# Performance work log

Measured on AMD Instinct MI355X. Metric: run time of the kernel, lower is better.

## Reference

```python
import jax, jax.numpy as jnp
import numpy as np

NHEADS = 8
MIN_DEPTH = 0.5
MAX_DEPTH = 100.0


def _gather(img, xi, yi, nb, W, H):
    valid = (xi >= 0) & (xi < W) & (yi >= 0) & (yi < H)
    xc = jnp.clip(xi, 0, W - 1)
    yc = jnp.clip(yi, 0, H - 1)
    vals = img[nb, :, yc, xc]  # (N,Ho,Wo,C) - advanced idx dims come first
    return vals * valid[..., None].astype(img.dtype)


def grid_sample(img, grid, mode='bilinear'):
    # img: (N,C,H,W), grid: (N,Ho,Wo,2) in [-1,1], zeros padding, align_corners=True
    N, C, H, W = img.shape
    gx = (grid[..., 0] + 1.0) * 0.5 * (W - 1)
    gy = (grid[..., 1] + 1.0) * 0.5 * (H - 1)
    nb = jnp.arange(N)[:, None, None]
    if mode == 'nearest':
        out = _gather(img, jnp.round(gx).astype(jnp.int32), jnp.round(gy).astype(jnp.int32), nb, W, H)
    else:
        x0 = jnp.floor(gx); y0 = jnp.floor(gy)
        wx = (gx - x0)[..., None]; wy = (gy - y0)[..., None]
        x0i = x0.astype(jnp.int32); y0i = y0.astype(jnp.int32)
        g00 = _gather(img, x0i, y0i, nb, W, H)
        g01 = _gather(img, x0i + 1, y0i, nb, W, H)
        g10 = _gather(img, x0i, y0i + 1, nb, W, H)
        g11 = _gather(img, x0i + 1, y0i + 1, nb, W, H)
        out = (1 - wy) * ((1 - wx) * g00 + wx * g01) + wy * ((1 - wx) * g10 + wx * g11)
    return jnp.transpose(out, (0, 3, 1, 2))  # (N,C,Ho,Wo)


def _avg3(x):
    # 3x3 avg pool, stride 1, reflect pad 1 (output same HxW)
    xp = jnp.pad(x, ((0, 0), (0, 0), (1, 1), (1, 1)), mode='reflect')
    return jax.lax.reduce_window(xp, 0.0, jax.lax.add, (1, 1, 3, 3), (1, 1, 1, 1), 'VALID') / 9.0


def ssim_loss(x, y, C1=1e-4, C2=9e-4):
    mx, my = _avg3(x), _avg3(y)
    sx = _avg3(x * x) - mx * mx
    sy = _avg3(y * y) - my * my
    sxy = _avg3(x * y) - mx * my
    num = (2 * mx * my + C1) * (2 * sxy + C2)
    den = (mx * mx + my * my + C1) * (sx + sy + C2)
    return jnp.clip((1.0 - num / den) * 0.5, 0.0, 1.0)


def prepare_b(x):
    d, c, h, w = x.shape
    return x.transpose(0, 2, 3, 1).reshape(d, h * w, c)  # (seq=d, batch=h*w, c)


def layer_norm(x, g, b, eps=1e-5):
    m = x.mean(-1, keepdims=True)
    v = ((x - m) ** 2).mean(-1, keepdims=True)
    return (x - m) * jax.lax.rsqrt(v + eps) * g + b


def attention(q_in, kv_in, w_qkv, b_qkv, w_o, b_o):
    # q_in: (Lq,B,C), kv_in: (Lk,B,C)
    C = q_in.shape[-1]
    hd = C // NHEADS
    q = q_in @ w_qkv[:C].T + b_qkv[:C]
    kv = kv_in @ w_qkv[C:].T + b_qkv[C:]
    k, v = jnp.split(kv, 2, axis=-1)
    Lq, B = q.shape[0], q.shape[1]
    Lk = k.shape[0]
    q = (q * (hd ** -0.5)).reshape(Lq, B, NHEADS, hd)
    k = k.reshape(Lk, B, NHEADS, hd)
    v = v.reshape(Lk, B, NHEADS, hd)
    attn = jnp.einsum('wnhc,vnhc->nhwv', q, k)  # (B,H,Lq,Lk)
    p = jax.nn.softmax(attn, axis=-1)
    out = jnp.einsum('nhwv,vnhc->wnhc', p, v).reshape(Lq, B, C)
    out = out @ w_o.T + b_o
    raw = attn.sum(axis=1)  # (B,Lq,Lk)
    return out, raw


def _forward(feat1, feat2, coords, sa_in_w, sa_in_b, sa_out_w, sa_out_b, sa_ln_g, sa_ln_b,
             ca_in_w, ca_in_b, ca_out_w, ca_out_b, ca_ln_g, ca_ln_b, num_bins):
    bs, C, h, w = feat1.shape
    cg = jnp.where(coords < -1.0, -2.0, coords)
    cg = jnp.where(cg > 1.0, 2.0, cg)
    rep_feat2 = jnp.broadcast_to(feat2, (num_bins, C, h, w))
    warped = grid_sample(rep_feat2, cg, 'bilinear')  # (num_bins,C,h,w)
    ones = jnp.ones((num_bins, 1, h, w), feat1.dtype)
    warped_mask = grid_sample(ones, cg, 'nearest')
    # SSIM cost volume (no-grad side outputs)
    x = jnp.broadcast_to(feat1, warped.shape)
    ssim_volume = jax.lax.stop_gradient(ssim_loss(x, warped).mean(axis=1)[None])  # (1,num_bins,h,w)
    idx = jnp.argmin(ssim_volume, axis=1)  # (1,h,w)
    depth = jnp.exp(np.float32(np.log(MIN_DEPTH)) + np.float32(np.log(MAX_DEPTH / MIN_DEPTH)) * idx.astype(feat1.dtype) / (num_bins - 1))
    lowest_cost = 1.0 / depth
    f1 = prepare_b(feat1)   # (bs, h*w, C)
    f2 = prepare_b(warped)  # (num_bins, h*w, C)
    raw = None
    L = sa_in_w.shape[0]
    for i in range(L):
        f1n = layer_norm(f1, sa_ln_g[i], sa_ln_b[i])
        o, _ = attention(f1n, f1n, sa_in_w[i], sa_in_b[i], sa_out_w[i], sa_out_b[i])
        f1 = f1 + o
        f1n = layer_norm(f1, ca_ln_g[i], ca_ln_b[i])
        f2n = layer_norm(f2, ca_ln_g[i], ca_ln_b[i])
        o, raw = attention(f1n, f2n, ca_in_w[i], ca_in_b[i], ca_out_w[i], ca_out_b[i])
        f1 = f1 + o
    attn_weight = raw.reshape(bs, h, w, num_bins)
    return attn_weight, warped_mask, lowest_cost, ssim_volume


def setup_inputs():
    key = jax.random.key(0)
    ks = jax.random.split(key, 16)
    C, L, NB, H, W = 128, 6, 64, 48, 160
    s = 0.02
    return {
        'feat1': jax.random.normal(ks[0], (1, C, H, W), jnp.float32),
        'feat2': jax.random.normal(ks[1], (1, C, H, W), jnp.float32),
        'coords': jax.random.uniform(ks[2], (NB, H, W, 2), jnp.float32) * 2.4 - 1.2,
        'sa_in_w': jax.random.normal(ks[3], (L, 3 * C, C), jnp.float32) * s,
        'sa_in_b': jax.random.normal(ks[4], (L, 3 * C), jnp.float32) * s,
        'sa_out_w': jax.random.normal(ks[5], (L, C, C), jnp.float32) * s,
        'sa_out_b': jax.random.normal(ks[6], (L, C), jnp.float32) * s,
        'sa_ln_g': jnp.ones((L, C), jnp.float32),
        'sa_ln_b': jnp.zeros((L, C), jnp.float32),
        'ca_in_w': jax.random.normal(ks[7], (L, 3 * C, C), jnp.float32) * s,
        'ca_in_b': jax.random.normal(ks[8], (L, 3 * C), jnp.float32) * s,
        'ca_out_w': jax.random.normal(ks[9], (L, C, C), jnp.float32) * s,
        'ca_out_b': jax.random.normal(ks[10], (L, C), jnp.float32) * s,
        'ca_ln_g': jnp.ones((L, C), jnp.float32),
        'ca_ln_b': jnp.zeros((L, C), jnp.float32),
        'num_bins': NB,
    }


def reference(feat1, feat2, coords, sa_in_w, sa_in_b, sa_out_w, sa_out_b, sa_ln_g, sa_ln_b,
              ca_in_w, ca_in_b, ca_out_w, ca_out_b, ca_ln_g, ca_ln_b, num_bins):
    return _forward(feat1, feat2, coords, sa_in_w, sa_in_b, sa_out_w, sa_out_b, sa_ln_g, sa_ln_b,
                    ca_in_w, ca_in_b, ca_out_w, ca_out_b, ca_ln_g, ca_ln_b, num_bins)
```

## Files before the change

### kernel.cpp

```cpp
#include <hip/hip_runtime.h>

constexpr int kH  = 48;
constexpr int kW  = 160;
constexpr int kP  = 7680;
constexpr int kC  = 128;
constexpr int kNB = 64;
constexpr int kNH = 8;
constexpr int kNL = 6;

constexpr long long OFF_F1T = 0;
constexpr long long OFF_F2T = 983040;
constexpr long long OFF_F2  = 1966080;
constexpr long long OFF_MU  = OFF_F2 + 62914560LL;
constexpr long long OFF_SIG = OFF_MU + 491520LL;
constexpr long long OFF_WTS = OFF_SIG + 491520LL;
constexpr int WSA2 = 0;
constexpr int WQ2  = 8192;
constexpr int WKU  = 16384;
constexpr int WV2  = 24576;
constexpr int WO2  = 32768;
constexpr int BSA  = 40960;
constexpr int BQ   = 41088;
constexpr int BK   = 41216;
constexpr int BV   = 41344;
constexpr int WTS_STRIDE = 41472;

constexpr long long OUT_ATT  = 0;
constexpr long long OUT_MASK = 491520;
constexpr long long OUT_LC   = 983040;
constexpr long long OUT_SSIM = 990720;

typedef _Float16 h2v __attribute__((ext_vector_type(2)));
typedef __fp16 p2v __attribute__((ext_vector_type(2)));
typedef float f2v __attribute__((ext_vector_type(2)));
union U32H2 { unsigned u; h2v h; };
union U32P2 { unsigned u; p2v h; };

__device__ __forceinline__ float fdot2(unsigned a, unsigned b, float c) {
  U32H2 ua; ua.u = a; U32H2 ub; ub.u = b;
  return __builtin_amdgcn_fdot2(ua.h, ub.h, c, false);
}
__device__ __forceinline__ unsigned pkrtz(float a, float b) {
  U32P2 t; t.h = __builtin_amdgcn_cvt_pkrtz(a, b); return t.u;
}
__device__ __forceinline__ f2v h2f(unsigned u) {
  U32P2 t; t.u = u; f2v r; r.x = (float)t.h.x; r.y = (float)t.h.y; return r;
}
__device__ __forceinline__ unsigned short f2h(float x) {
  U32P2 t; t.h = __builtin_amdgcn_cvt_pkrtz(x, 0.f); return (unsigned short)(t.u & 0xffffu);
}
__device__ __forceinline__ void wb() {
  __asm__ __volatile__("" ::: "memory");
  __builtin_amdgcn_wave_barrier();
  __asm__ __volatile__("" ::: "memory");
}

__global__ void k_transpose(const float* __restrict__ feat1, const float* __restrict__ feat2,
                            float* __restrict__ f1t, float* __restrict__ f2t) {
  int idx = blockIdx.x * 256 + threadIdx.x;
  int pix = idx >> 7, c = idx & 127;
  f1t[idx] = feat1[c * kP + pix];
  f2t[idx] = feat2[c * kP + pix];
}

__device__ __forceinline__ float redsum128(float v, float* red2) {
#pragma unroll
  for (int off = 32; off > 0; off >>= 1) v += __shfl_xor(v, off);
  int t = threadIdx.x;
  if ((t & 63) == 0) red2[t >> 6] = v;
  __syncthreads();
  float r = red2[0] + red2[1];
  __syncthreads();
  return r;
}

__global__ __launch_bounds__(128) void k_fold(
    const float* __restrict__ saw_, const float* __restrict__ sab_,
    const float* __restrict__ sow_, const float* __restrict__ sob_,
    const float* __restrict__ slg_, const float* __restrict__ slb_,
    const float* __restrict__ caw_, const float* __restrict__ cab_,
    const float* __restrict__ clg_, const float* __restrict__ clb_,
    const float* __restrict__ cow_, float* __restrict__ wts) {
  int i = blockIdx.x >> 7, d = blockIdx.x & 127, c = threadIdx.x;
  const float* saw = saw_ + (long long)i * 384 * kC;
  const float* sab = sab_ + i * 384;
  const float* sow = sow_ + i * kC * kC;
  const float* sob = sob_ + i * kC;
  const float* slg = slg_ + i * kC;
  const float* slb = slb_ + i * kC;
  const float* caw = caw_ + (long long)i * 384 * kC;
  const float* cab = cab_ + i * 384;
  const float* clg = clg_ + i * kC;
  const float* clb = clb_ + i * kC;
  const float* cow = cow_ + i * kC * kC;
  float* WL = wts + (long long)i * WTS_STRIDE;
  __shared__ float red2[2];

  int jstd = (c >> 3) * 1024 + d * 8 + (c & 7);

  float acc = 0.f;
  for (int m = 0; m < kC; m++) acc += sow[d * kC + m] * saw[(256 + m) * kC + c];
  float t1 = redsum128(acc * slb[c] + sow[d * kC + c] * sab[256 + c], red2);
  if (c == 0) WL[BSA + d] = t1 + sob[d];
  ((unsigned short*)(WL + WSA2))[jstd] = f2h(acc * slg[c]);

  float wq = caw[d * kC + c];
  float t2 = redsum128(wq * clb[c], red2);
  if (c == 0) WL[BQ + d] = 0.25f * (t2 + cab[d]);
  ((unsigned short*)(WL + WQ2))[jstd] = f2h(0.25f * wq * clg[c]);

  float wk = caw[(kC + d) * kC + c];
  float t3 = redsum128(wk * clb[c], red2);
  if (c == 0) WL[BK + d] = t3 + cab[kC + d];
  {
    int h = d >> 4, o = d & 15;
    ((unsigned short*)(WL + WKU))[h * 2048 + c * 16 + o] = f2h(wk * clg[c]);
  }

  float wv = caw[(2 * kC + d) * kC + c];
  float t4 = redsum128(wv * clb[c], red2);
  if (c == 0) WL[BV + d] = t4 + cab[2 * kC + d];
  ((unsigned short*)(WL + WV2))[jstd] = f2h(wv * clg[c]);

  ((unsigned short*)(WL + WO2))[jstd] = f2h(cow[d * kC + c]);
}

__global__ __launch_bounds__(256) void k_warp(const float* __restrict__ f2t,
                                              const float* __restrict__ coords,
                                              float* __restrict__ F2, float* __restrict__ mu,
                                              float* __restrict__ sig, float* __restrict__ maskout) {
  int wave = threadIdx.x >> 6, lane = threadIdx.x & 63;
  int pix = blockIdx.x * 4 + wave;
  int b = blockIdx.y;
  long long bp = (long long)b * kP + pix;
  float cx = coords[bp * 2], cy = coords[bp * 2 + 1];
  cx = (cx < -1.f) ? -2.f : cx;
  cx = (cx > 1.f) ? 2.f : cx;
  cy = (cy < -1.f) ? -2.f : cy;
  cy = (cy > 1.f) ? 2.f : cy;
  float gx = (cx + 1.f) * 0.5f * (float)(kW - 1);
  float gy = (cy + 1.f) * 0.5f * (float)(kH - 1);
  float x0f = floorf(gx), y0f = floorf(gy);
  float wx = gx - x0f, wy = gy - y0f;
  int x0 = (int)x0f, y0 = (int)y0f;
  int x1 = x0 + 1, y1 = y0 + 1;
  float vx0 = (x0 >= 0 && x0 < kW) ? 1.f : 0.f;
  float vx1 = (x1 >= 0 && x1 < kW) ? 1.f : 0.f;
  float vy0 = (y0 >= 0 && y0 < kH) ? 1.f : 0.f;
  float vy1 = (y1 >= 0 && y1 < kH) ? 1.f : 0.f;
  int x0c = min(max(x0, 0), kW - 1), x1c = min(max(x1, 0), kW - 1);
  int y0c = min(max(y0, 0), kH - 1), y1c = min(max(y1, 0), kH - 1);
  float w00 = (1.f - wy) * (1.f - wx) * vx0 * vy0;
  float w01 = (1.f - wy) * wx * vx1 * vy0;
  float w10 = wy * (1.f - wx) * vx0 * vy1;
  float w11 = wy * wx * vx1 * vy1;
  const float2* r00 = (const float2*)(f2t + (y0c * kW + x0c) * kC);
  const float2* r01 = (const float2*)(f2t + (y0c * kW + x1c) * kC);
  const float2* r10 = (const float2*)(f2t + (y1c * kW + x0c) * kC);
  const float2* r11 = (const float2*)(f2t + (y1c * kW + x1c) * kC);
  float2 g00 = r00[lane], g01 = r01[lane], g10 = r10[lane], g11 = r11[lane];
  float v0 = w00 * g00.x + w01 * g01.x + w10 * g10.x + w11 * g11.x;
  float v1 = w00 * g00.y + w01 * g01.y + w10 * g10.y + w11 * g11.y;
  float s = v0 + v1, s2 = v0 * v0 + v1 * v1;
#pragma unroll
  for (int off = 32; off > 0; off >>= 1) {
    s += __shfl_xor(s, off);
    s2 += __shfl_xor(s2, off);
  }
  float m = s * (1.f / 128.f);
  float var = s2 * (1.f / 128.f) - m * m;
  float rs = rsqrtf(var + 1e-5f);
  float2 o;
  o.x = (v0 - m) * rs;
  o.y = (v1 - m) * rs;
  ((float2*)(F2 + bp * kC))[lane] = o;
  if (lane == 0) {
    mu[bp] = m;
    sig[bp] = sqrtf(var + 1e-5f);
    int xi = (int)rintf(gx), yi = (int)rintf(gy);
    maskout[bp] = (xi >= 0 && xi < kW && yi >= 0 && yi < kH) ? 1.f : 0.f;
  }
}

__global__ __launch_bounds__(256) void k_ssim(const float* __restrict__ f1t,
                                              const float* __restrict__ F2,
                                              const float* __restrict__ mu,
                                              const float* __restrict__ sig,
                                              float* __restrict__ ssimout) {
  const int lane = threadIdx.x & 63;
  const int y = blockIdx.x * 4 + (threadIdx.x >> 6);
  const int b = blockIdx.y;
  const int ym = (y == 0) ? 1 : y - 1;
  const int yp = (y == kH - 1) ? kH - 2 : y + 1;
  const long long bb = (long long)b * kP;
  const float* f1m = f1t + (ym * kW) * kC + 2 * lane;
  const float* f10 = f1t + (y * kW) * kC + 2 * lane;
  const float* f1p = f1t + (yp * kW) * kC + 2 * lane;
  const float* F2m = F2 + (bb + ym * kW) * kC + 2 * lane;
  const float* F20 = F2 + (bb + y * kW) * kC + 2 * lane;
  const float* F2p = F2 + (bb + yp * kW) * kC + 2 * lane;
  const float* mum = mu + bb + ym * kW;
  const float* mu0 = mu + bb + y * kW;
  const float* mup = mu + bb + yp * kW;
  const float* sgm = sig + bb + ym * kW;
  const float* sg0 = sig + bb + y * kW;
  const float* sgp = sig + bb + yp * kW;
  float* outrow = ssimout + bb + y * kW;

  f2v C[3][5];

  auto colsum = [&](int x, f2v* Cc) {
    f2v am = *(const f2v*)(f1m + (size_t)x * kC);
    f2v a0 = *(const f2v*)(f10 + (size_t)x * kC);
    f2v ap = *(const f2v*)(f1p + (size_t)x * kC);
    f2v fm = *(const f2v*)(F2m + (size_t)x * kC);
    f2v f0 = *(const f2v*)(F20 + (size_t)x * kC);
    f2v fp = *(const f2v*)(F2p + (size_t)x * kC);
    f2v wm = fm * sgm[x] + mum[x];
    f2v w0 = f0 * sg0[x] + mu0[x];
    f2v wp = fp * sgp[x] + mup[x];
    Cc[0] = am + a0 + ap;
    Cc[1] = wm + w0 + wp;
    Cc[2] = am * am + a0 * a0 + ap * ap;
    Cc[3] = wm * wm + w0 * w0 + wp * wp;
    Cc[4] = am * wm + a0 * w0 + ap * wp;
  };

  auto emit = [&](int xo, f2v s0, f2v s1, f2v s2, f2v s3, f2v s4) {
    const float inv9 = 1.f / 9.f;
    f2v mx = s0 * inv9, my = s1 * inv9;
    f2v vx = s2 * inv9 - mx * mx;
    f2v vy = s3 * inv9 - my * my;
    f2v vxy = s4 * inv9 - mx * my;
    f2v num = (2.f * mx * my + 1e-4f) * (2.f * vxy + 9e-4f);
    f2v den = (mx * mx + my * my + 1e-4f) * (vx + vy + 9e-4f);
    f2v val = (1.f - num / den) * 0.5f;
    float t = fminf(fmaxf(val.x, 0.f), 1.f) + fminf(fmaxf(val.y, 0.f), 1.f);
#pragma unroll
    for (int o = 32; o > 0; o >>= 1) t += __shfl_xor(t, o);
    if (lane == 0) outrow[xo] = t * (1.f / 128.f);
  };

  colsum(0, C[0]);
  colsum(1, C[1]);
  emit(0, C[0][0] + 2.f * C[1][0], C[0][1] + 2.f * C[1][1], C[0][2] + 2.f * C[1][2],
       C[0][3] + 2.f * C[1][3], C[0][4] + 2.f * C[1][4]);
#pragma unroll 3
  for (int x = 2; x < kW; ++x) {
    colsum(x, C[x % 3]);
    emit(x - 1, C[0][0] + C[1][0] + C[2][0], C[0][1] + C[1][1] + C[2][1],
         C[0][2] + C[1][2] + C[2][2], C[0][3] + C[1][3] + C[2][3],
         C[0][4] + C[1][4] + C[2][4]);
  }
  emit(kW - 1, C[0][0] + 2.f * C[2][0], C[0][1] + 2.f * C[2][1], C[0][2] + 2.f * C[2][2],
       C[0][3] + 2.f * C[2][3], C[0][4] + 2.f * C[2][4]);
}

__global__ __launch_bounds__(256) void k_argmin(const float* __restrict__ ssim,
                                                float* __restrict__ lc) {
  int pix = blockIdx.x * 256 + threadIdx.x;
  float best = ssim[pix];
  int bi = 0;
  for (int b = 1; b < kNB; b++) {
    float v = ssim[b * kP + pix];
    if (v < best) { best = v; bi = b; }
  }
  float depth = expf(-0.69314718f + (5.2983174f * (float)bi) / 63.0f);
  lc[pix] = 1.f / depth;
}


__device__ __forceinline__ f2v gemmW(int l, const unsigned* __restrict__ inb,
                                     const unsigned* __restrict__ W, float b0, float b1) {
  float a0 = b0, a1 = b1, c0 = 0.f, c1 = 0.f;
  const unsigned* wp = W + l * 8;
#pragma unroll
  for (int j = 0; j < 16; j += 2) {
    uint4 inA = *(const uint4*)(inb + 4 * j);
    uint4 inB = *(const uint4*)(inb + 4 * j + 4);
    uint4 wa = *(const uint4*)(wp + j * 512);
    uint4 wc = *(const uint4*)(wp + j * 512 + 4);
    uint4 wa2 = *(const uint4*)(wp + j * 512 + 512);
    uint4 wc2 = *(const uint4*)(wp + j * 512 + 516);
    a0 = fdot2(inA.x, wa.x, a0);  a0 = fdot2(inA.y, wa.y, a0);
    a0 = fdot2(inA.z, wa.z, a0);  a0 = fdot2(inA.w, wa.w, a0);
    a1 = fdot2(inA.x, wc.x, a1);  a1 = fdot2(inA.y, wc.y, a1);
    a1 = fdot2(inA.z, wc.z, a1);  a1 = fdot2(inA.w, wc.w, a1);
    c0 = fdot2(inB.x, wa2.x, c0); c0 = fdot2(inB.y, wa2.y, c0);
    c0 = fdot2(inB.z, wa2.z, c0); c0 = fdot2(inB.w, wa2.w, c0);
    c1 = fdot2(inB.x, wc2.x, c1); c1 = fdot2(inB.y, wc2.y, c1);
    c1 = fdot2(inB.z, wc2.z, c1); c1 = fdot2(inB.w, wc2.w, c1);
  }
  f2v r; r.x = a0 + c0; r.y = a1 + c1; return r;
}

__device__ __forceinline__ void ln_store(int l, f2v X, unsigned* xhq) {
  float s = X.x + X.y, s2 = X.x * X.x + X.y * X.y;
#pragma unroll
  for (int o = 32; o > 0; o >>= 1) { s += __shfl_xor(s, o); s2 += __shfl_xor(s2, o); }
  float m = s * 0.0078125f;
  float var = s2 * 0.0078125f - m * m;
  float rs = rsqrtf(var + 1e-5f);
  xhq[l] = pkrtz((X.x - m) * rs, (X.y - m) * rs);
}

__global__ __launch_bounds__(64) void k_attn(const float* __restrict__ F2g,
                                             const float* __restrict__ f1t,
                                             const float* __restrict__ wts,
                                             const float* __restrict__ cab_out,
                                             float* __restrict__ attn_out) {
  __shared__ __align__(16) unsigned F2s[64 * 64];
  __shared__ __align__(16) unsigned upb[512];
  __shared__ __align__(16) unsigned xhq[64];

  const int l = threadIdx.x;
  const int pix = blockIdx.x;

  {
#pragma unroll 4
    for (int r = 0; r < 64; ++r) {
      float2 v = *(const float2*)(F2g + ((long long)r * kP + pix) * kC + 2 * l);
      F2s[r * 64 + (l ^ (4 * (r & 15)))] = pkrtz(v.x, v.y);
    }
  }
  f2v X;
  { float2 xv = ((const float2*)(f1t + (long long)pix * kC))[l]; X.x = xv.x; X.y = xv.y; }
  wb();

  float chsum = 0.f;
  float* pf = (float*)upb;

  for (int ly = 0; ly < kNL; ++ly) {
    const float* WL = wts + (long long)ly * WTS_STRIDE;

    ln_store(l, X, xhq);
    wb();
    {
      float2 bv = ((const float2*)(WL + BSA))[l];
      f2v o = gemmW(l, xhq, (const unsigned*)(WL + WSA2), bv.x, bv.y);
      X += o;
    }
    wb();
    ln_store(l, X, xhq);
    wb();
    f2v q;
    {
      float2 bv = ((const float2*)(WL + BQ))[l];
      q = gemmW(l, xhq, (const unsigned*)(WL + WQ2), bv.x, bv.y);
    }
    if (ly == kNL - 1) {
      float2 bk = ((const float2*)(WL + BK))[l];
      float cp = q.x * bk.x + q.y * bk.y;
#pragma unroll
      for (int o = 32; o > 0; o >>= 1) cp += __shfl_xor(cp, o);
      chsum = cp;
    }
    xhq[l] = pkrtz(q.x, q.y);
    wb();

    {
      const unsigned* KU = (const unsigned*)(WL + WKU);
#pragma unroll
      for (int h = 0; h < kNH; ++h) {
        uint4 q0 = *(const uint4*)(xhq + h * 8);
        uint4 q1 = *(const uint4*)(xhq + h * 8 + 4);
        const unsigned* w0 = KU + (h * 128 + 2 * l) * 8;
        uint4 a0 = ((const uint4*)w0)[0], a1 = ((const uint4*)w0)[1];
        uint4 b0 = ((const uint4*)w0)[2], b1 = ((const uint4*)w0)[3];
        float u0 = 0.f, u1 = 0.f, u2 = 0.f, u3 = 0.f;
        u0 = fdot2(q0.x, a0.x, u0); u0 = fdot2(q0.y, a0.y, u0);
        u0 = fdot2(q0.z, a0.z, u0); u0 = fdot2(q0.w, a0.w, u0);
        u2 = fdot2(q1.x, a1.x, u2); u2 = fdot2(q1.y, a1.y, u2);
        u2 = fdot2(q1.z, a1.z, u2); u2 = fdot2(q1.w, a1.w, u2);
        u1 = fdot2(q0.x, b0.x, u1); u1 = fdot2(q0.y, b0.y, u1);
        u1 = fdot2(q0.z, b0.z, u1); u1 = fdot2(q0.w, b0.w, u1);
        u3 = fdot2(q1.x, b1.x, u3); u3 = fdot2(q1.y, b1.y, u3);
        u3 = fdot2(q1.z, b1.z, u3); u3 = fdot2(q1.w, b1.w, u3);
        upb[h * 64 + l] = pkrtz(u0 + u2, u1 + u3);
      }
    }
    wb();

    float sc[8] = {0, 0, 0, 0, 0, 0, 0, 0};
    {
      const unsigned* f2row = F2s + l * 64;
      const int sw = 4 * (l & 15);
#pragma unroll 4
      for (int j = 0; j < 16; ++j) {
        uint4 fv = *(const uint4*)(f2row + ((4 * j) ^ sw));
#pragma unroll
        for (int h = 0; h < kNH; ++h) {
          uint4 uv = *(const uint4*)(upb + h * 64 + 4 * j);
          sc[h] = fdot2(fv.x, uv.x, sc[h]);
          sc[h] = fdot2(fv.y, uv.y, sc[h]);
          sc[h] = fdot2(fv.z, uv.z, sc[h]);
          sc[h] = fdot2(fv.w, uv.w, sc[h]);
        }
      }
    }
    if (ly == kNL - 1) {
      float r = sc[0] + sc[1] + sc[2] + sc[3] + sc[4] + sc[5] + sc[6] + sc[7] + chsum;
      attn_out[(long long)pix * 64 + l] = r;
      return;
    }
    wb();
    {
      float pv[8];
#pragma unroll
      for (int h = 0; h < kNH; ++h) {
        float mx = sc[h];
#pragma unroll
        for (int o = 32; o > 0; o >>= 1) mx = fmaxf(mx, __shfl_xor(mx, o));
        float e = __expf(sc[h] - mx);
        float sm = e;
#pragma unroll
        for (int o = 32; o > 0; o >>= 1) sm += __shfl_xor(sm, o);
        pv[h] = e / sm;
      }
      *(float4*)(pf + l * 8) = make_float4(pv[0], pv[1], pv[2], pv[3]);
      *(float4*)(pf + l * 8 + 4) = make_float4(pv[4], pv[5], pv[6], pv[7]);
    }
    wb();
    {
      const int half = l >> 5, lb = l & 31;
      f2v wA[8], wB[8];
#pragma unroll
      for (int h = 0; h < kNH; ++h) { wA[h] = (f2v)0.f; wB[h] = (f2v)0.f; }
#pragma unroll 2
      for (int t = 0; t < 32; ++t) {
        int b = half * 32 + t;
        uint2 fv = *(const uint2*)(F2s + b * 64 + ((2 * lb) ^ (4 * (b & 15))));
        f2v fA = h2f(fv.x), fB = h2f(fv.y);
        float4 pA = *(const float4*)(pf + b * 8);
        float4 pB = *(const float4*)(pf + b * 8 + 4);
        wA[0] += fA * pA.x; wB[0] += fB * pA.x;
        wA[1] += fA * pA.y; wB[1] += fB * pA.y;
        wA[2] += fA * pA.z; wB[2] += fB * pA.z;
        wA[3] += fA * pA.w; wB[3] += fB * pA.w;
        wA[4] += fA * pB.x; wB[4] += fB * pB.x;
        wA[5] += fA * pB.y; wB[5] += fB * pB.y;
        wA[6] += fA * pB.z; wB[6] += fB * pB.z;
        wA[7] += fA * pB.w; wB[7] += fB * pB.w;
      }
#pragma unroll
      for (int h = 0; h < kNH; ++h) {
        wA[h].x += __shfl_xor(wA[h].x, 32);
        wA[h].y += __shfl_xor(wA[h].y, 32);
        wB[h].x += __shfl_xor(wB[h].x, 32);
        wB[h].y += __shfl_xor(wB[h].y, 32);
      }
      wb();
#pragma unroll
      for (int hh = 0; hh < 4; ++hh) {
        int h = half * 4 + hh;
        uint2 pk;
        pk.x = pkrtz(wA[h].x, wA[h].y);
        pk.y = pkrtz(wB[h].x, wB[h].y);
        *(uint2*)(upb + h * 64 + ((2 * lb) ^ (4 * h))) = pk;
      }
    }
    wb();
    {
      const int h = l >> 3;
      const unsigned* wrow = upb + h * 64;
      const unsigned* WV = (const unsigned*)(WL + WV2) + l * 8;
      float2 bv = ((const float2*)(WL + BV))[l];
      float a0 = bv.x, a1 = bv.y, c0 = 0.f, c1 = 0.f;
      const int sw = 4 * h;
#pragma unroll
      for (int j = 0; j < 16; j += 2) {
        uint4 inA = *(const uint4*)(wrow + ((4 * j) ^ sw));
        uint4 inB = *(const uint4*)(wrow + ((4 * j + 4) ^ sw));
        uint4 wa = *(const uint4*)(WV + j * 512);
        uint4 wc = *(const uint4*)(WV + j * 512 + 4);
        uint4 wa2 = *(const uint4*)(WV + j * 512 + 512);
        uint4 wc2 = *(const uint4*)(WV + j * 512 + 516);
        a0 = fdot2(inA.x, wa.x, a0);  a0 = fdot2(inA.y, wa.y, a0);
        a0 = fdot2(inA.z, wa.z, a0);  a0 = fdot2(inA.w, wa.w, a0);
        a1 = fdot2(inA.x, wc.x, a1);  a1 = fdot2(inA.y, wc.y, a1);
        a1 = fdot2(inA.z, wc.z, a1);  a1 = fdot2(inA.w, wc.w, a1);
        c0 = fdot2(inB.x, wa2.x, c0); c0 = fdot2(inB.y, wa2.y, c0);
        c0 = fdot2(inB.z, wa2.z, c0); c0 = fdot2(inB.w, wa2.w, c0);
        c1 = fdot2(inB.x, wc2.x, c1); c1 = fdot2(inB.y, wc2.y, c1);
        c1 = fdot2(inB.z, wc2.z, c1); c1 = fdot2(inB.w, wc2.w, c1);
      }
      xhq[l] = pkrtz(a0 + c0, a1 + c1);
    }
    wb();
    {
      float2 bv = ((const float2*)(cab_out + ly * kC))[l];
      f2v o = gemmW(l, xhq, (const unsigned*)(WL + WO2), bv.x, bv.y);
      X += o;
    }
    wb();
  }
}

extern "C" void kernel_launch(void* const* d_in, const int* in_sizes, int n_in, void* d_out,
                              int out_size, void* d_ws, size_t ws_size, hipStream_t stream) {
  (void)in_sizes; (void)n_in; (void)out_size; (void)ws_size;
  const float* feat1 = (const float*)d_in[0];
  const float* feat2 = (const float*)d_in[1];
  const float* coords = (const float*)d_in[2];
  const float* sa_in_w = (const float*)d_in[3];
  const float* sa_in_b = (const float*)d_in[4];
  const float* sa_out_w = (const float*)d_in[5];
  const float* sa_out_b = (const float*)d_in[6];
  const float* sa_ln_g = (const float*)d_in[7];
  const float* sa_ln_b = (const float*)d_in[8];
  const float* ca_in_w = (const float*)d_in[9];
  const float* ca_in_b = (const float*)d_in[10];
  const float* ca_out_w = (const float*)d_in[11];
  const float* ca_out_b = (const float*)d_in[12];
  const float* ca_ln_g = (const float*)d_in[13];
  const float* ca_ln_b = (const float*)d_in[14];

  float* out = (float*)d_out;
  float* ws = (float*)d_ws;
  float* f1t = ws + OFF_F1T;
  float* f2t = ws + OFF_F2T;
  float* F2 = ws + OFF_F2;
  float* mu = ws + OFF_MU;
  float* sig = ws + OFF_SIG;
  float* wts = ws + OFF_WTS;

  float* att = out + OUT_ATT;
  float* mask = out + OUT_MASK;
  float* lc = out + OUT_LC;
  float* ssim = out + OUT_SSIM;

  k_transpose<<<3840, 256, 0, stream>>>(feat1, feat2, f1t, f2t);
  k_fold<<<kNL * 128, 128, 0, stream>>>(sa_in_w, sa_in_b, sa_out_w, sa_out_b, sa_ln_g, sa_ln_b,
                                        ca_in_w, ca_in_b, ca_ln_g, ca_ln_b, ca_out_w, wts);
  dim3 g1(1920, 64);
  k_warp<<<g1, 256, 0, stream>>>(f2t, coords, F2, mu, sig, mask);
  dim3 g2(12, 64);
  k_ssim<<<g2, 256, 0, stream>>>(f1t, F2, mu, sig, ssim);
  k_argmin<<<30, 256, 0, stream>>>(ssim, lc);
  k_attn<<<kP, 64, 0, stream>>>(F2, f1t, wts, ca_out_b, att);
}
```

Measured before the change: 789.7 us.

## Use two waves per pixel in attention kernel with one output channel per thread

The attention kernel now runs 128 threads (two waves) per pixel instead of one wave. Each thread owns a single channel instead of two, and the heads are split across the two waves for the score, softmax and weighted-sum phases. The goal is to halve the per-thread serial work and register pressure and to raise latency hiding through more waves, via launch bounds of 128 threads and 4 blocks. In exchange, the cheap intra-wave barriers become __syncthreads with shared-memory reductions for LayerNorm and the final sum, and the weight matrices are read with a different per-thread layout.

```diff
diff --git a/kernel.cpp b/kernel.cpp
--- a/kernel.cpp
+++ b/kernel.cpp
@@ -48,11 +48,6 @@
 }
 __device__ __forceinline__ unsigned short f2h(float x) {
   U32P2 t; t.h = __builtin_amdgcn_cvt_pkrtz(x, 0.f); return (unsigned short)(t.u & 0xffffu);
-}
-__device__ __forceinline__ void wb() {
-  __asm__ __volatile__("" ::: "memory");
-  __builtin_amdgcn_wave_barrier();
-  __asm__ __volatile__("" ::: "memory");
 }
 
 __global__ void k_transpose(const float* __restrict__ feat1, const float* __restrict__ feat2,
@@ -270,229 +265,187 @@
 }
 
 
-__device__ __forceinline__ f2v gemmW(int l, const unsigned* __restrict__ inb,
-                                     const unsigned* __restrict__ W, float b0, float b1) {
-  float a0 = b0, a1 = b1, c0 = 0.f, c1 = 0.f;
-  const unsigned* wp = W + l * 8;
-#pragma unroll
-  for (int j = 0; j < 16; j += 2) {
-    uint4 inA = *(const uint4*)(inb + 4 * j);
-    uint4 inB = *(const uint4*)(inb + 4 * j + 4);
-    uint4 wa = *(const uint4*)(wp + j * 512);
-    uint4 wc = *(const uint4*)(wp + j * 512 + 4);
-    uint4 wa2 = *(const uint4*)(wp + j * 512 + 512);
-    uint4 wc2 = *(const uint4*)(wp + j * 512 + 516);
-    a0 = fdot2(inA.x, wa.x, a0);  a0 = fdot2(inA.y, wa.y, a0);
-    a0 = fdot2(inA.z, wa.z, a0);  a0 = fdot2(inA.w, wa.w, a0);
-    a1 = fdot2(inA.x, wc.x, a1);  a1 = fdot2(inA.y, wc.y, a1);
-    a1 = fdot2(inA.z, wc.z, a1);  a1 = fdot2(inA.w, wc.w, a1);
-    c0 = fdot2(inB.x, wa2.x, c0); c0 = fdot2(inB.y, wa2.y, c0);
-    c0 = fdot2(inB.z, wa2.z, c0); c0 = fdot2(inB.w, wa2.w, c0);
-    c1 = fdot2(inB.x, wc2.x, c1); c1 = fdot2(inB.y, wc2.y, c1);
-    c1 = fdot2(inB.z, wc2.z, c1); c1 = fdot2(inB.w, wc2.w, c1);
-  }
-  f2v r; r.x = a0 + c0; r.y = a1 + c1; return r;
-}
-
-__device__ __forceinline__ void ln_store(int l, f2v X, unsigned* xhq) {
-  float s = X.x + X.y, s2 = X.x * X.x + X.y * X.y;
-#pragma unroll
-  for (int o = 32; o > 0; o >>= 1) { s += __shfl_xor(s, o); s2 += __shfl_xor(s2, o); }
-  float m = s * 0.0078125f;
-  float var = s2 * 0.0078125f - m * m;
-  float rs = rsqrtf(var + 1e-5f);
-  xhq[l] = pkrtz((X.x - m) * rs, (X.y - m) * rs);
-}
-
-__global__ __launch_bounds__(64) void k_attn(const float* __restrict__ F2g,
-                                             const float* __restrict__ f1t,
-                                             const float* __restrict__ wts,
-                                             const float* __restrict__ cab_out,
-                                             float* __restrict__ attn_out) {
+__device__ __forceinline__ float gemm128(const unsigned* __restrict__ xh32,
+                                         const unsigned* __restrict__ W, int d, float bias) {
+  float a0 = bias, a1 = 0.f, a2 = 0.f, a3 = 0.f;
+  const unsigned* wp = W + d * 4;
+#pragma unroll
+  for (int ch = 0; ch < 16; ++ch) {
+    uint4 wv = *(const uint4*)(wp + ch * 512);
+    uint4 xv = *(const uint4*)(xh32 + ch * 4);
+    a0 = fdot2(xv.x, wv.x, a0);
+    a1 = fdot2(xv.y, wv.y, a1);
+    a2 = fdot2(xv.z, wv.z, a2);
+    a3 = fdot2(xv.w, wv.w, a3);
+  }
+  return (a0 + a1) + (a2 + a3);
+}
+
+__global__ __launch_bounds__(128, 4) void k_attn(const float* __restrict__ F2g,
+                                                 const float* __restrict__ f1t,
+                                                 const float* __restrict__ wts,
+                                                 const float* __restrict__ cab_out,
+                                                 float* __restrict__ attn_out) {
   __shared__ __align__(16) unsigned F2s[64 * 64];
   __shared__ __align__(16) unsigned upb[512];
-  __shared__ __align__(16) unsigned xhq[64];
-
-  const int l = threadIdx.x;
+  __shared__ __align__(16) unsigned xh[64];
+  __shared__ __align__(16) unsigned q2[64];
+  __shared__ float2 redf[2];
+  __shared__ float redc[2];
+  __shared__ float rawp[128];
+
+  const int t = threadIdx.x;
+  const int w = t >> 6, l = t & 63;
   const int pix = blockIdx.x;
-
-  {
-#pragma unroll 4
-    for (int r = 0; r < 64; ++r) {
-      float2 v = *(const float2*)(F2g + ((long long)r * kP + pix) * kC + 2 * l);
-      F2s[r * 64 + (l ^ (4 * (r & 15)))] = pkrtz(v.x, v.y);
-    }
-  }
-  f2v X;
-  { float2 xv = ((const float2*)(f1t + (long long)pix * kC))[l]; X.x = xv.x; X.y = xv.y; }
-  wb();
+  unsigned short* xh16 = (unsigned short*)xh;
+  unsigned short* q16 = (unsigned short*)q2;
+  unsigned short* ub16 = (unsigned short*)upb;
+  float* pf = (float*)upb;
+
+  for (int r = w * 32; r < w * 32 + 32; ++r) {
+    float2 v = *(const float2*)(F2g + ((long long)r * kP + pix) * kC + 2 * l);
+    F2s[r * 64 + (l ^ (4 * (r & 15)))] = pkrtz(v.x, v.y);
+  }
+  float X = f1t[(long long)pix * kC + t];
+  __syncthreads();
 
   float chsum = 0.f;
-  float* pf = (float*)upb;
 
   for (int ly = 0; ly < kNL; ++ly) {
     const float* WL = wts + (long long)ly * WTS_STRIDE;
 
-    ln_store(l, X, xhq);
-    wb();
-    {
-      float2 bv = ((const float2*)(WL + BSA))[l];
-      f2v o = gemmW(l, xhq, (const unsigned*)(WL + WSA2), bv.x, bv.y);
-      X += o;
-    }
-    wb();
-    ln_store(l, X, xhq);
-    wb();
-    f2v q;
-    {
-      float2 bv = ((const float2*)(WL + BQ))[l];
-      q = gemmW(l, xhq, (const unsigned*)(WL + WQ2), bv.x, bv.y);
-    }
-    if (ly == kNL - 1) {
-      float2 bk = ((const float2*)(WL + BK))[l];
-      float cp = q.x * bk.x + q.y * bk.y;
-#pragma unroll
-      for (int o = 32; o > 0; o >>= 1) cp += __shfl_xor(cp, o);
-      chsum = cp;
-    }
-    xhq[l] = pkrtz(q.x, q.y);
-    wb();
-
+    {
+      float s = X, s2 = X * X;
+#pragma unroll
+      for (int o = 32; o > 0; o >>= 1) { s += __shfl_xor(s, o); s2 += __shfl_xor(s2, o); }
+      if (l == 0) redf[w] = make_float2(s, s2);
+      __syncthreads();
+      float2 tot = redf[0], t1 = redf[1];
+      float m = (tot.x + t1.x) * 0.0078125f;
+      float var = (tot.y + t1.y) * 0.0078125f - m * m;
+      xh16[t] = f2h((X - m) * rsqrtf(var + 1e-5f));
+      __syncthreads();
+    }
+    X += gemm128(xh, (const unsigned*)(WL + WSA2), t, WL[BSA + t]);
+    {
+      float s = X, s2 = X * X;
+#pragma unroll
+      for (int o = 32; o > 0; o >>= 1) { s += __shfl_xor(s, o); s2 += __shfl_xor(s2, o); }
+      if (l == 0) redf[w] = make_float2(s, s2);
+      __syncthreads();
+      float2 tot = redf[0], t1 = redf[1];
+      float m = (tot.x + t1.x) * 0.0078125f;
+      float var = (tot.y + t1.y) * 0.0078125f - m * m;
+      xh16[t] = f2h((X - m) * rsqrtf(var + 1e-5f));
+      __syncthreads();
+    }
+    {
+      float qv = gemm128(xh, (const unsigned*)(WL + WQ2), t, WL[BQ + t]);
+      q16[t] = f2h(qv);
+      if (ly == kNL - 1) {
+        float cp = qv * WL[BK + t];
+#pragma unroll
+        for (int o = 32; o > 0; o >>= 1) cp += __shfl_xor(cp, o);
+        if (l == 0) redc[w] = cp;
+      }
+      __syncthreads();
+      if (ly == kNL - 1) chsum = redc[0] + redc[1];
+    }
     {
       const unsigned* KU = (const unsigned*)(WL + WKU);
 #pragma unroll
       for (int h = 0; h < kNH; ++h) {
-        uint4 q0 = *(const uint4*)(xhq + h * 8);
-        uint4 q1 = *(const uint4*)(xhq + h * 8 + 4);
-        const unsigned* w0 = KU + (h * 128 + 2 * l) * 8;
-        uint4 a0 = ((const uint4*)w0)[0], a1 = ((const uint4*)w0)[1];
-        uint4 b0 = ((const uint4*)w0)[2], b1 = ((const uint4*)w0)[3];
+        uint4 w0 = *(const uint4*)(KU + h * 1024 + t * 8);
+        uint4 w1 = *(const uint4*)(KU + h * 1024 + t * 8 + 4);
+        uint4 qa = *(const uint4*)(q2 + h * 8);
+        uint4 qb = *(const uint4*)(q2 + h * 8 + 4);
         float u0 = 0.f, u1 = 0.f, u2 = 0.f, u3 = 0.f;
-        u0 = fdot2(q0.x, a0.x, u0); u0 = fdot2(q0.y, a0.y, u0);
-        u0 = fdot2(q0.z, a0.z, u0); u0 = fdot2(q0.w, a0.w, u0);
-        u2 = fdot2(q1.x, a1.x, u2); u2 = fdot2(q1.y, a1.y, u2);
-        u2 = fdot2(q1.z, a1.z, u2); u2 = fdot2(q1.w, a1.w, u2);
-        u1 = fdot2(q0.x, b0.x, u1); u1 = fdot2(q0.y, b0.y, u1);
-        u1 = fdot2(q0.z, b0.z, u1); u1 = fdot2(q0.w, b0.w, u1);
-        u3 = fdot2(q1.x, b1.x, u3); u3 = fdot2(q1.y, b1.y, u3);
-        u3 = fdot2(q1.z, b1.z, u3); u3 = fdot2(q1.w, b1.w, u3);
-        upb[h * 64 + l] = pkrtz(u0 + u2, u1 + u3);
-      }
-    }
-    wb();
-
-    float sc[8] = {0, 0, 0, 0, 0, 0, 0, 0};
+        u0 = fdot2(qa.x, w0.x, u0); u1 = fdot2(qa.y, w0.y, u1);
+        u2 = fdot2(qa.z, w0.z, u2); u3 = fdot2(qa.w, w0.w, u3);
+        u0 = fdot2(qb.x, w1.x, u0); u1 = fdot2(qb.y, w1.y, u1);
+        u2 = fdot2(qb.z, w1.z, u2); u3 = fdot2(qb.w, w1.w, u3);
+        ub16[h * 128 + t] = f2h((u0 + u1) + (u2 + u3));
+      }
+      __syncthreads();
+    }
+    float sc[4] = {0, 0, 0, 0};
     {
       const unsigned* f2row = F2s + l * 64;
       const int sw = 4 * (l & 15);
+      const int hb = 4 * w;
 #pragma unroll 4
       for (int j = 0; j < 16; ++j) {
         uint4 fv = *(const uint4*)(f2row + ((4 * j) ^ sw));
 #pragma unroll
-        for (int h = 0; h < kNH; ++h) {
-          uint4 uv = *(const uint4*)(upb + h * 64 + 4 * j);
-          sc[h] = fdot2(fv.x, uv.x, sc[h]);
-          sc[h] = fdot2(fv.y, uv.y, sc[h]);
-          sc[h] = fdot2(fv.z, uv.z, sc[h]);
-          sc[h] = fdot2(fv.w, uv.w, sc[h]);
+        for (int k = 0; k < 4; ++k) {
+          uint4 uv = *(const uint4*)(upb + (hb + k) * 64 + 4 * j);
+          sc[k] = fdot2(fv.x, uv.x, sc[k]);
+          sc[k] = fdot2(fv.y, uv.y, sc[k]);
+          sc[k] = fdot2(fv.z, uv.z, sc[k]);
+          sc[k] = fdot2(fv.w, uv.w, sc[k]);
         }
       }
     }
     if (ly == kNL - 1) {
-      float r = sc[0] + sc[1] + sc[2] + sc[3] + sc[4] + sc[5] + sc[6] + sc[7] + chsum;
-      attn_out[(long long)pix * 64 + l] = r;
+      rawp[w * 64 + l] = sc[0] + sc[1] + sc[2] + sc[3];
+      __syncthreads();
+      if (t < 64) attn_out[(long long)pix * 64 + t] = rawp[t] + rawp[64 + t] + chsum;
       return;
     }
-    wb();
-    {
-      float pv[8];
-#pragma unroll
-      for (int h = 0; h < kNH; ++h) {
-        float mx = sc[h];
+    __syncthreads();
+    {
+      float pv[4];
+#pragma unroll
+      for (int k = 0; k < 4; ++k) {
+        float mx = sc[k];
 #pragma unroll
         for (int o = 32; o > 0; o >>= 1) mx = fmaxf(mx, __shfl_xor(mx, o));
-        float e = __expf(sc[h] - mx);
+        float e = __expf(sc[k] - mx);
         float sm = e;
 #pragma unroll
         for (int o = 32; o > 0; o >>= 1) sm += __shfl_xor(sm, o);
-        pv[h] = e / sm;
-      }
-      *(float4*)(pf + l * 8) = make_float4(pv[0], pv[1], pv[2], pv[3]);
-      *(float4*)(pf + l * 8 + 4) = make_float4(pv[4], pv[5], pv[6], pv[7]);
-    }
-    wb();
-    {
-      const int half = l >> 5, lb = l & 31;
-      f2v wA[8], wB[8];
-#pragma unroll
-      for (int h = 0; h < kNH; ++h) { wA[h] = (f2v)0.f; wB[h] = (f2v)0.f; }
-#pragma unroll 2
-      for (int t = 0; t < 32; ++t) {
-        int b = half * 32 + t;
-        uint2 fv = *(const uint2*)(F2s + b * 64 + ((2 * lb) ^ (4 * (b & 15))));
-        f2v fA = h2f(fv.x), fB = h2f(fv.y);
-        float4 pA = *(const float4*)(pf + b * 8);
-        float4 pB = *(const float4*)(pf + b * 8 + 4);
-        wA[0] += fA * pA.x; wB[0] += fB * pA.x;
-        wA[1] += fA * pA.y; wB[1] += fB * pA.y;
-        wA[2] += fA * pA.z; wB[2] += fB * pA.z;
-        wA[3] += fA * pA.w; wB[3] += fB * pA.w;
-        wA[4] += fA * pB.x; wB[4] += fB * pB.x;
-        wA[5] += fA * pB.y; wB[5] += fB * pB.y;
-        wA[6] += fA * pB.z; wB[6] += fB * pB.z;
-        wA[7] += fA * pB.w; wB[7] += fB * pB.w;
-      }
-#pragma unroll
-      for (int h = 0; h < kNH; ++h) {
-        wA[h].x += __shfl_xor(wA[h].x, 32);
-        wA[h].y += __shfl_xor(wA[h].y, 32);
-        wB[h].x += __shfl_xor(wB[h].x, 32);
-        wB[h].y += __shfl_xor(wB[h].y, 32);
-      }
-      wb();
-#pragma unroll
-      for (int hh = 0; hh < 4; ++hh) {
-        int h = half * 4 + hh;
-        uint2 pk;
-        pk.x = pkrtz(wA[h].x, wA[h].y);
-        pk.y = pkrtz(wB[h].x, wB[h].y);
-        *(uint2*)(upb + h * 64 + ((2 * lb) ^ (4 * h))) = pk;
-      }
-    }
-    wb();
-    {
-      const int h = l >> 3;
-      const unsigned* wrow = upb + h * 64;
-      const unsigned* WV = (const unsigned*)(WL + WV2) + l * 8;
-      float2 bv = ((const float2*)(WL + BV))[l];
-      float a0 = bv.x, a1 = bv.y, c0 = 0.f, c1 = 0.f;
+        pv[k] = e / sm;
+      }
+      *(float4*)(pf + l * 8 + 4 * w) = make_float4(pv[0], pv[1], pv[2], pv[3]);
+    }
+    __syncthreads();
+    {
+      const int hb = 4 * w;
+      f2v acc0 = (f2v)0.f, acc1 = (f2v)0.f, acc2 = (f2v)0.f, acc3 = (f2v)0.f;
+#pragma unroll 4
+      for (int b = 0; b < 64; ++b) {
+        f2v f = h2f(F2s[b * 64 + (l ^ (4 * (b & 15)))]);
+        float4 pv = *(const float4*)(pf + b * 8 + hb);
+        acc0 += f * pv.x;
+        acc1 += f * pv.y;
+        acc2 += f * pv.z;
+        acc3 += f * pv.w;
+      }
+      __syncthreads();
+      upb[(hb + 0) * 64 + (l ^ (4 * (hb + 0)))] = pkrtz(acc0.x, acc0.y);
+      upb[(hb + 1) * 64 + (l ^ (4 * (hb + 1)))] = pkrtz(acc1.x, acc1.y);
+      upb[(hb + 2) * 64 + (l ^ (4 * (hb + 2)))] = pkrtz(acc2.x, acc2.y);
+      upb[(hb + 3) * 64 + (l ^ (4 * (hb + 3)))] = pkrtz(acc3.x, acc3.y);
+      __syncthreads();
+    }
+    {
+      const int h = t >> 4;
+      const unsigned* WV = (const unsigned*)(WL + WV2) + t * 4;
+      float a0 = WL[BV + t], a1 = 0.f, a2 = 0.f, a3 = 0.f;
       const int sw = 4 * h;
 #pragma unroll
-      for (int j = 0; j < 16; j += 2) {
-        uint4 inA = *(const uint4*)(wrow + ((4 * j) ^ sw));
-        uint4 inB = *(const uint4*)(wrow + ((4 * j + 4) ^ sw));
-        uint4 wa = *(const uint4*)(WV + j * 512);
-        uint4 wc = *(const uint4*)(WV + j * 512 + 4);
-        uint4 wa2 = *(const uint4*)(WV + j * 512 + 512);
-        uint4 wc2 = *(const uint4*)(WV + j * 512 + 516);
-        a0 = fdot2(inA.x, wa.x, a0);  a0 = fdot2(inA.y, wa.y, a0);
-        a0 = fdot2(inA.z, wa.z, a0);  a0 = fdot2(inA.w, wa.w, a0);
-        a1 = fdot2(inA.x, wc.x, a1);  a1 = fdot2(inA.y, wc.y, a1);
-        a1 = fdot2(inA.z, wc.z, a1);  a1 = fdot2(inA.w, wc.w, a1);
-        c0 = fdot2(inB.x, wa2.x, c0); c0 = fdot2(inB.y, wa2.y, c0);
-        c0 = fdot2(inB.z, wa2.z, c0); c0 = fdot2(inB.w, wa2.w, c0);
-        c1 = fdot2(inB.x, wc2.x, c1); c1 = fdot2(inB.y, wc2.y, c1);
-        c1 = fdot2(inB.z, wc2.z, c1); c1 = fdot2(inB.w, wc2.w, c1);
-      }
-      xhq[l] = pkrtz(a0 + c0, a1 + c1);
-    }
-    wb();
-    {
-      float2 bv = ((const float2*)(cab_out + ly * kC))[l];
-      f2v o = gemmW(l, xhq, (const unsigned*)(WL + WO2), bv.x, bv.y);
-      X += o;
-    }
-    wb();
+      for (int ch = 0; ch < 16; ++ch) {
+        uint4 wv = *(const uint4*)(WV + ch * 512);
+        uint4 iv = *(const uint4*)(upb + h * 64 + ((4 * ch) ^ sw));
+        a0 = fdot2(iv.x, wv.x, a0);
+        a1 = fdot2(iv.y, wv.y, a1);
+        a2 = fdot2(iv.z, wv.z, a2);
+        a3 = fdot2(iv.w, wv.w, a3);
+      }
+      xh16[t] = f2h((a0 + a1) + (a2 + a3));
+      __syncthreads();
+    }
+    X += gemm128(xh, (const unsigned*)(WL + WO2), t, cab_out[ly * kC + t]);
   }
 }
 
@@ -537,5 +490,5 @@
   dim3 g2(12, 64);
   k_ssim<<<g2, 256, 0, stream>>>(f1t, F2, mu, sig, ssim);
   k_argmin<<<30, 256, 0, stream>>>(ssim, lc);
-  k_attn<<<kP, 64, 0, stream>>>(F2, f1t, wts, ca_out_b, att);
-}
+  k_attn<<<kP, 128, 0, stream>>>(F2, f1t, wts, ca_out_b, att);
+}
```

Measured after the change: 1.044 ms. 1.32x slower.

## Compute per-head attention scores with MFMA 32x32x16 instead of fdot2 loops

Applied to the files above, without the earlier changes.

Replaces the per-lane fdot2 loop that computes the 64 bins × 8 heads score matrix with two MFMA 32x32x16 f16 instructions per K-chunk. Each lane's B column is indexed by head via mrow&7, so columns 8–31 are redundant copies. The softmax is restructured around the MFMA output layout: max and sum are reduced in registers plus one cross-half shuffle, and only lanes with mrow<8 write probabilities to shared memory. This cuts dot-product instruction count and cross-lane shuffles. In exchange, 75% of the MFMA work is wasted on duplicate columns and the result layout needs remapping through shared memory.

```diff
diff --git a/kernel.cpp b/kernel.cpp
--- a/kernel.cpp
+++ b/kernel.cpp
@@ -33,6 +33,8 @@
 typedef _Float16 h2v __attribute__((ext_vector_type(2)));
 typedef __fp16 p2v __attribute__((ext_vector_type(2)));
 typedef float f2v __attribute__((ext_vector_type(2)));
+typedef __fp16 h8 __attribute__((ext_vector_type(8)));
+typedef float fx16 __attribute__((ext_vector_type(16)));
 union U32H2 { unsigned u; h2v h; };
 union U32P2 { unsigned u; p2v h; };
 
@@ -329,6 +331,9 @@
 
   float chsum = 0.f;
   float* pf = (float*)upb;
+  const int mrow = l & 31;
+  const int kg = l >> 5;
+  const int rbase = 4 * kg;
 
   for (int ly = 0; ly < kNL; ++ly) {
     const float* WL = wts + (long long)ly * WTS_STRIDE;
@@ -381,44 +386,60 @@
     }
     wb();
 
-    float sc[8] = {0, 0, 0, 0, 0, 0, 0, 0};
-    {
-      const unsigned* f2row = F2s + l * 64;
-      const int sw = 4 * (l & 15);
-#pragma unroll 4
-      for (int j = 0; j < 16; ++j) {
-        uint4 fv = *(const uint4*)(f2row + ((4 * j) ^ sw));
-#pragma unroll
-        for (int h = 0; h < kNH; ++h) {
-          uint4 uv = *(const uint4*)(upb + h * 64 + 4 * j);
-          sc[h] = fdot2(fv.x, uv.x, sc[h]);
-          sc[h] = fdot2(fv.y, uv.y, sc[h]);
-          sc[h] = fdot2(fv.z, uv.z, sc[h]);
-          sc[h] = fdot2(fv.w, uv.w, sc[h]);
+    fx16 acc0 = (fx16)0.f, acc1 = (fx16)0.f;
+    {
+      const int hn = mrow & 7;
+      const int sw = 4 * (mrow & 15);
+#pragma unroll
+      for (int kc = 0; kc < 8; ++kc) {
+        const int cp = kc * 8 + kg * 4;
+        h8 Bv = *(const h8*)(upb + hn * 64 + cp);
+        h8 A0 = *(const h8*)(F2s + mrow * 64 + (cp ^ sw));
+        h8 A1 = *(const h8*)(F2s + (mrow + 32) * 64 + (cp ^ sw));
+        acc0 = __builtin_amdgcn_mfma_f32_32x32x16_f16(A0, Bv, acc0, 0, 0, 0);
+        acc1 = __builtin_amdgcn_mfma_f32_32x32x16_f16(A1, Bv, acc1, 0, 0, 0);
+      }
+    }
+    if (ly == kNL - 1) {
+      wb();
+      if (mrow < 8) {
+#pragma unroll
+        for (int r = 0; r < 16; ++r) {
+          int row = (r & 3) + 8 * (r >> 2) + rbase;
+          pf[mrow * 64 + row] = acc0[r];
+          pf[mrow * 64 + 32 + row] = acc1[r];
         }
       }
-    }
-    if (ly == kNL - 1) {
-      float r = sc[0] + sc[1] + sc[2] + sc[3] + sc[4] + sc[5] + sc[6] + sc[7] + chsum;
-      attn_out[(long long)pix * 64 + l] = r;
+      wb();
+      float rsum = chsum;
+#pragma unroll
+      for (int h = 0; h < kNH; ++h) rsum += pf[h * 64 + l];
+      attn_out[(long long)pix * 64 + l] = rsum;
       return;
     }
-    wb();
-    {
-      float pv[8];
-#pragma unroll
-      for (int h = 0; h < kNH; ++h) {
-        float mx = sc[h];
-#pragma unroll
-        for (int o = 32; o > 0; o >>= 1) mx = fmaxf(mx, __shfl_xor(mx, o));
-        float e = __expf(sc[h] - mx);
-        float sm = e;
-#pragma unroll
-        for (int o = 32; o > 0; o >>= 1) sm += __shfl_xor(sm, o);
-        pv[h] = e / sm;
-      }
-      *(float4*)(pf + l * 8) = make_float4(pv[0], pv[1], pv[2], pv[3]);
-      *(float4*)(pf + l * 8 + 4) = make_float4(pv[4], pv[5], pv[6], pv[7]);
+    {
+      float mx = acc0[0];
+#pragma unroll
+      for (int r = 0; r < 16; ++r) { mx = fmaxf(mx, acc0[r]); mx = fmaxf(mx, acc1[r]); }
+      mx = fmaxf(mx, __shfl_xor(mx, 32));
+      float pv0[16], pv1[16];
+      float sm = 0.f;
+#pragma unroll
+      for (int r = 0; r < 16; ++r) {
+        pv0[r] = __expf(acc0[r] - mx); sm += pv0[r];
+        pv1[r] = __expf(acc1[r] - mx); sm += pv1[r];
+      }
+      sm += __shfl_xor(sm, 32);
+      float inv = 1.f / sm;
+      wb();
+      if (mrow < 8) {
+#pragma unroll
+        for (int r = 0; r < 16; ++r) {
+          int row = (r & 3) + 8 * (r >> 2) + rbase;
+          pf[row * 8 + mrow] = pv0[r] * inv;
+          pf[(32 + row) * 8 + mrow] = pv1[r] * inv;
+        }
+      }
     }
     wb();
     {
```

Result: slower. 914.6 us (+15.8%).
